# Performance work log

Hardware: AMD Instinct MI355X
Metric: run time of the kernel (lower is better)

The kernel has to match this reference:

```python
import jax, jax.numpy as jnp
import numpy as np

DIM = 768
HEADS = 8
HEAD_DIM = DIM // HEADS
SCALE = HEAD_DIM ** -0.5
EPS = 1e-5


def layernorm(x, gamma, beta):
    mu = jnp.mean(x, axis=-1, keepdims=True)
    var = jnp.mean((x - mu) ** 2, axis=-1, keepdims=True)
    return (x - mu) * jax.lax.rsqrt(var + EPS) * gamma + beta


def setup_inputs() -> dict:
    key = jax.random.key(0)
    ks = jax.random.split(key, 12)
    B, L, M, D = 8, 1024, 1024, DIM
    s = D ** -0.5
    return {
        "x": jax.random.normal(ks[0], (B, L, D), jnp.float32),
        "context": jax.random.normal(ks[1], (B, M, D), jnp.float32),
        "Wq": jax.random.normal(ks[2], (D, D), jnp.float32) * s,
        "bq": jnp.zeros((D,), jnp.float32),
        "Wkv": jax.random.normal(ks[3], (D, 2 * D), jnp.float32) * s,
        "bkv": jnp.zeros((2 * D,), jnp.float32),
        "Wp": jax.random.normal(ks[4], (D, D), jnp.float32) * s,
        "bp": jnp.zeros((D,), jnp.float32),
        "g1": jnp.ones((D,), jnp.float32),
        "b1": jnp.zeros((D,), jnp.float32),
        "g2": jnp.ones((D,), jnp.float32),
        "b2": jnp.zeros((D,), jnp.float32),
    }


def reference(x, context, Wq, bq, Wkv, bkv, Wp, bp, g1, b1, g2, b2):
    B, L, D = x.shape
    M = context.shape[1]
    Hp = Wp_ = int(L ** 0.5)
    x_n = layernorm(x, g1, b1)
    c_n = layernorm(context, g2, b2)
    q = (x_n @ Wq + bq).reshape(B, L, HEADS, HEAD_DIM).transpose(0, 2, 1, 3)  # bhld
    kv = (c_n @ Wkv + bkv).reshape(B, M, 2, HEADS, HEAD_DIM).transpose(2, 0, 3, 1, 4)
    k, v = kv[0], kv[1]  # bhmd
    attn = jnp.einsum("bhld,bhmd->bhlm", q, k) * SCALE
    w = jax.nn.softmax(attn, axis=-1)
    attn_map = w.mean(axis=1).sum(axis=-1).reshape(B, Hp, Wp_)
    out = jnp.einsum("bhlm,bhmd->bhld", w, v).transpose(0, 2, 1, 3).reshape(B, L, D)
    out = out @ Wp + bp
    # dropout is identity in eval mode (training=False)
    return out + x, attn_map
```

## Files before the change

kernel.cpp:

```cpp
#include <hip/hip_runtime.h>

typedef unsigned short u16;
typedef short bf16x8 __attribute__((ext_vector_type(8)));
typedef float f32x4 __attribute__((ext_vector_type(4)));
typedef unsigned short u16x8 __attribute__((ext_vector_type(8)));
typedef unsigned short u16x4 __attribute__((ext_vector_type(4)));

union bfr { unsigned int u[4]; bf16x8 v; };

__device__ __forceinline__ u16 f2bf(float f) {
    unsigned int u = __builtin_bit_cast(unsigned int, f);
    u = (u + 0x7fffu + ((u >> 16) & 1u)) >> 16;
    return (u16)u;
}

__device__ __forceinline__ unsigned int cvtpk(float lo, float hi) {
    unsigned int r;
    asm("v_cvt_pk_bf16_f32 %0, %1, %2" : "=v"(r) : "v"(lo), "v"(hi));
    return r;
}

__device__ __forceinline__ void gload16(const u16* src, u16* lds_dst) {
    __builtin_amdgcn_global_load_lds(
        (const __attribute__((address_space(1))) unsigned int*)src,
        (__attribute__((address_space(3))) unsigned int*)lds_dst, 16, 0, 0);
}

__global__ __launch_bounds__(256) void prep_ln_k(
    const float* __restrict__ x, const float* __restrict__ ctx,
    const float* __restrict__ g1, const float* __restrict__ b1,
    const float* __restrict__ g2, const float* __restrict__ b2,
    const float* __restrict__ Wq, const float* __restrict__ Wkv,
    const float* __restrict__ Wp,
    u16* __restrict__ xn, u16* __restrict__ cn,
    u16* __restrict__ WqT, u16* __restrict__ WkvT, u16* __restrict__ WpT)
{
    const int id = blockIdx.x;
    const int t = threadIdx.x;
    if (id >= 4096) {
        __shared__ float T[64][65];
        int t2 = id - 4096;
        const float* src; u16* dst; int lds, k0, n0;
        if (t2 < 288) { src = Wkv; dst = WkvT; lds = 1536; k0 = (t2 / 24) * 64; n0 = (t2 % 24) * 64; }
        else if (t2 < 432) { int u = t2 - 288; src = Wq; dst = WqT; lds = 768; k0 = (u / 12) * 64; n0 = (u % 12) * 64; }
        else { int u = t2 - 432; src = Wp; dst = WpT; lds = 768; k0 = (u / 12) * 64; n0 = (u % 12) * 64; }
        const int rr = t >> 4, c4 = (t & 15) * 4;
        #pragma unroll
        for (int it = 0; it < 4; it++) {
            int r = rr + it * 16;
            f32x4 v = *(const f32x4*)&src[(long)(k0 + r) * lds + n0 + c4];
            #pragma unroll
            for (int j = 0; j < 4; j++) T[c4 + j][r] = v[j];
        }
        __syncthreads();
        #pragma unroll
        for (int it = 0; it < 4; it++) {
            int r = rr + it * 16;
            u16x4 w;
            #pragma unroll
            for (int j = 0; j < 4; j++) w[j] = f2bf(T[r][c4 + j]);
            *(u16x4*)&dst[(long)(n0 + r) * 768 + k0 + c4] = w;
        }
        return;
    }
    const int lane = t & 63, w = t >> 6;
    const int row = id * 4 + w;
    const float* src; const float* g; const float* b; u16* dst;
    if (row < 8192) { src = x + (long)row * 768; g = g1; b = b1; dst = xn + (long)row * 768; }
    else { int r = row - 8192; src = ctx + (long)r * 768; g = g2; b = b2; dst = cn + (long)r * 768; }

    const int c0 = lane * 4;
    f32x4 v0 = *(const f32x4*)&src[c0];
    f32x4 v1 = *(const f32x4*)&src[c0 + 256];
    f32x4 v2 = *(const f32x4*)&src[c0 + 512];
    float s = (v0[0] + v0[1] + v0[2] + v0[3]) + (v1[0] + v1[1] + v1[2] + v1[3])
            + (v2[0] + v2[1] + v2[2] + v2[3]);
    #pragma unroll
    for (int o = 32; o; o >>= 1) s += __shfl_xor(s, o);
    const float mu = s * (1.0f / 768.0f);
    float q = 0.f;
    #pragma unroll
    for (int j = 0; j < 4; j++) { float d = v0[j] - mu; q += d * d; }
    #pragma unroll
    for (int j = 0; j < 4; j++) { float d = v1[j] - mu; q += d * d; }
    #pragma unroll
    for (int j = 0; j < 4; j++) { float d = v2[j] - mu; q += d * d; }
    #pragma unroll
    for (int o = 32; o; o >>= 1) q += __shfl_xor(q, o);
    const float rs = rsqrtf(q * (1.0f / 768.0f) + 1e-5f);

    f32x4 ga0 = *(const f32x4*)&g[c0],       ba0 = *(const f32x4*)&b[c0];
    f32x4 ga1 = *(const f32x4*)&g[c0 + 256], ba1 = *(const f32x4*)&b[c0 + 256];
    f32x4 ga2 = *(const f32x4*)&g[c0 + 512], ba2 = *(const f32x4*)&b[c0 + 512];
    u16x4 w0, w1, w2;
    #pragma unroll
    for (int j = 0; j < 4; j++) {
        w0[j] = f2bf((v0[j] - mu) * rs * ga0[j] + ba0[j]);
        w1[j] = f2bf((v1[j] - mu) * rs * ga1[j] + ba1[j]);
        w2[j] = f2bf((v2[j] - mu) * rs * ga2[j] + ba2[j]);
    }
    *(u16x4*)&dst[c0]       = w0;
    *(u16x4*)&dst[c0 + 256] = w1;
    *(u16x4*)&dst[c0 + 512] = w2;
}

__global__ __launch_bounds__(256) void qkv_k(
    const u16* __restrict__ xn, const u16* __restrict__ cn,
    const u16* __restrict__ WqT, const u16* __restrict__ WkvT,
    const float* __restrict__ bq, const float* __restrict__ bkv,
    u16* __restrict__ Qb, u16* __restrict__ Kb, u16* __restrict__ Vt)
{
    __shared__ u16 As[64 * 32];
    __shared__ u16 Bs[128 * 32];
    const int id = blockIdx.x;
    const int swz = (id & 7) * 288 + (id >> 3);
    const int tid = threadIdx.x, lane = tid & 63, wid = tid >> 6;
    const int wr = wid >> 1, wc = wid & 1;
    const int g = lane >> 4, i15 = lane & 15;

    const bool isQ = swz < 768;
    int rt, ct;
    const u16* A; const u16* Bt; const float* bias;
    if (isQ) { rt = swz / 6;  ct = swz % 6;  A = xn; Bt = WqT;  bias = bq; }
    else { int s2 = swz - 768; rt = s2 / 12; ct = s2 % 12; A = cn; Bt = WkvT; bias = bkv; }
    const int row0 = rt * 64, col0 = ct * 128;

    const u16* srcA; const u16* srcB[2]; int offA, offB[2];
    {
        int r = tid >> 2, sl = tid & 3;
        srcA = A + (long)(row0 + r) * 768 + ((sl ^ ((r >> 1) & 3)) << 3);
        offA = wid * 512 + lane * 8;
        #pragma unroll
        for (int c = 0; c < 2; c++) {
            int ch = c * 256 + tid;
            int rb = ch >> 2, slb = ch & 3;
            srcB[c] = Bt + (long)(col0 + rb) * 768 + ((slb ^ ((rb >> 1) & 3)) << 3);
            offB[c] = (c * 256 + wid * 64) * 8 + lane * 8;
        }
    }
    const int dA = wid * 512;
    int dB[2]; dB[0] = wid * 512; dB[1] = 2048 + wid * 512;

    int aoff[2], boff[4];
    #pragma unroll
    for (int m = 0; m < 2; m++) {
        int R = wr * 32 + m * 16 + i15;
        aoff[m] = R * 32 + ((g ^ ((R >> 1) & 3)) << 3);
    }
    #pragma unroll
    for (int n = 0; n < 4; n++) {
        int R = wc * 64 + n * 16 + i15;
        boff[n] = R * 32 + ((g ^ ((R >> 1) & 3)) << 3);
    }

    f32x4 acc[2][4] = {};
    for (int k0 = 0; k0 < 768; k0 += 32) {
        __syncthreads();
        gload16(srcA + k0, &As[dA]);
        #pragma unroll
        for (int c = 0; c < 2; c++)
            gload16(srcB[c] + k0, &Bs[dB[c]]);
        __syncthreads();
        bf16x8 av[2], bv[4];
        #pragma unroll
        for (int m = 0; m < 2; m++) av[m] = *(const bf16x8*)&As[aoff[m]];
        #pragma unroll
        for (int n = 0; n < 4; n++) bv[n] = *(const bf16x8*)&Bs[boff[n]];
        #pragma unroll
        for (int m = 0; m < 2; m++)
            #pragma unroll
            for (int n = 0; n < 4; n++)
                acc[m][n] = __builtin_amdgcn_mfma_f32_16x16x32_bf16(av[m], bv[n], acc[m][n], 0, 0, 0);
    }

    float bv4[4];
    #pragma unroll
    for (int n = 0; n < 4; n++) bv4[n] = bias[col0 + wc * 64 + n * 16 + i15];

    #pragma unroll
    for (int m = 0; m < 2; m++) {
        #pragma unroll
        for (int n = 0; n < 4; n++) {
            const int col = col0 + wc * 64 + n * 16 + i15;
            #pragma unroll
            for (int r = 0; r < 4; r++) {
                const int row = row0 + wr * 32 + m * 16 + g * 4 + r;
                float v = acc[m][n][r];
                if (isQ) {
                    v = (v + bv4[n]) * 0.14724444706f;
                    int b = row >> 10, l = row & 1023;
                    int h = col / 96, d = col % 96;
                    Qb[((long)(b * 8 + h) * 1024 + l) * 96 + d] = f2bf(v);
                } else {
                    v += bv4[n];
                    int b = row >> 10, mt = row & 1023;
                    if (col < 768) {
                        int h = col / 96, d = col % 96;
                        Kb[((long)(b * 8 + h) * 1024 + mt) * 96 + d] = f2bf(v);
                    } else {
                        int cc = col - 768;
                        int h = cc / 96, d = cc % 96;
                        Vt[((long)(b * 8 + h) * 96 + d) * 1024 + mt] = f2bf(v);
                    }
                }
            }
        }
    }
}

__global__ __launch_bounds__(256) void flash_k(
    const u16* __restrict__ Qb, const u16* __restrict__ Kb,
    const u16* __restrict__ Vt, u16* __restrict__ Ob)
{
    const int i = blockIdx.x;
    const int s8 = i >> 3;
    const int bh = (i & 7) * 8 + (s8 >> 4);
    const int qt = s8 & 15;
    const int tid = threadIdx.x, lane = tid & 63, wid = tid >> 6;
    const int g = lane >> 4, i15 = lane & 15;

    __shared__ u16 Ks[6144];
    __shared__ u16 Vs[2][6144];

    const long baseQK = (long)bh * 98304;
    const u16* Kt  = Kb + baseQK;
    const u16* Vtp = Vt + baseQK;

    bf16x8 qf[3];
    {
        const u16* qrow = Qb + baseQK + (long)(qt * 64 + wid * 16 + i15) * 96 + g * 8;
        qf[0] = *(const bf16x8*)(qrow);
        qf[1] = *(const bf16x8*)(qrow + 32);
        qf[2] = *(const bf16x8*)(qrow + 64);
    }

    int krd[4][3];
    #pragma unroll
    for (int n = 0; n < 4; n++) {
        int q4 = i15 >> 2, rr = i15 & 3, m = n >> 1;
        int R = (n & 1) ? (m * 32 + ((q4 ^ 2) << 3) + 4 + rr)
                        : (m * 32 + (q4 << 3) + rr);
        #pragma unroll
        for (int kd = 0; kd < 3; kd++)
            krd[n][kd] = kd * 2048 + R * 32 + ((g ^ ((R >> 3) & 3) ^ kd) << 3);
    }
    int vrd[6][2];
    #pragma unroll
    for (int n6 = 0; n6 < 6; n6++) {
        int row = n6 * 16 + i15;
        #pragma unroll
        for (int kk = 0; kk < 2; kk++)
            vrd[n6][kk] = row * 64 + ((kk * 32 + g * 8) ^ ((row & 7) << 3));
    }

    int kgo[3], kwr[3], vgo[3], vwr[3];
    #pragma unroll
    for (int it = 0; it < 3; it++) {
        int e = tid + it * 256;
        int r = e / 12, cEl = (e % 12) * 8;
        int kd = cEl >> 5, slot = (cEl >> 3) & 3;
        kgo[it] = r * 96 + cEl;
        kwr[it] = kd * 2048 + r * 32 + ((slot ^ ((r >> 3) & 3) ^ kd) << 3);
        int d = e >> 3, m8 = (e & 7) * 8;
        vgo[it] = d * 1024 + m8;
        vwr[it] = d * 64 + (m8 ^ ((d & 7) << 3));
    }

    u16x8 kreg[3], vreg[3];
    #pragma unroll
    for (int it = 0; it < 3; it++) {
        kreg[it] = *(const u16x8*)&Kt[kgo[it]];
        vreg[it] = *(const u16x8*)&Vtp[vgo[it]];
    }
    #pragma unroll
    for (int it = 0; it < 3; it++) {
        *(u16x8*)&Ks[kwr[it]] = kreg[it];
        *(u16x8*)&Vs[0][vwr[it]] = vreg[it];
    }

    f32x4 o[6] = {};
    float lsum = 0.f;
    int cur = 0;

    for (int t = 0; t < 16; t++) {
        __syncthreads();
        if (t < 15) {
            #pragma unroll
            for (int it = 0; it < 3; it++) {
                kreg[it] = *(const u16x8*)&Kt[(t + 1) * 6144 + kgo[it]];
                vreg[it] = *(const u16x8*)&Vtp[(t + 1) * 64 + vgo[it]];
            }
        }

        f32x4 s[4] = {};
        #pragma unroll
        for (int kd = 0; kd < 3; kd++) {
            #pragma unroll
            for (int n = 0; n < 4; n++) {
                bf16x8 kf = *(const bf16x8*)&Ks[krd[n][kd]];
                s[n] = __builtin_amdgcn_mfma_f32_16x16x32_bf16(kf, qf[kd], s[n], 0, 0, 0);
            }
        }
        __syncthreads();
        if (t < 15) {
            #pragma unroll
            for (int it = 0; it < 3; it++)
                *(u16x8*)&Ks[kwr[it]] = kreg[it];
        }

        unsigned int pk[4][2];
        #pragma unroll
        for (int n = 0; n < 4; n++) {
            float p0 = exp2f(s[n][0]), p1 = exp2f(s[n][1]);
            float p2 = exp2f(s[n][2]), p3 = exp2f(s[n][3]);
            lsum += (p0 + p1) + (p2 + p3);
            pk[n][0] = cvtpk(p0, p1);
            pk[n][1] = cvtpk(p2, p3);
        }

        #pragma unroll
        for (int kk = 0; kk < 2; kk++) {
            bfr pa;
            pa.u[0] = pk[kk * 2][0];
            pa.u[1] = pk[kk * 2][1];
            pa.u[2] = __shfl_xor(pk[kk * 2 + 1][0], 32);
            pa.u[3] = __shfl_xor(pk[kk * 2 + 1][1], 32);
            #pragma unroll
            for (int n6 = 0; n6 < 6; n6++) {
                bf16x8 vf = *(const bf16x8*)&Vs[cur][vrd[n6][kk]];
                o[n6] = __builtin_amdgcn_mfma_f32_16x16x32_bf16(pa.v, vf, o[n6], 0, 0, 0);
            }
        }

        if (t < 15) {
            #pragma unroll
            for (int it = 0; it < 3; it++)
                *(u16x8*)&Vs[cur ^ 1][vwr[it]] = vreg[it];
        }
        cur ^= 1;
    }

    lsum += __shfl_xor(lsum, 16);
    lsum += __shfl_xor(lsum, 32);
    float linv = 1.0f / lsum;

    const int b = bh >> 3, h = bh & 7;
    #pragma unroll
    for (int r = 0; r < 4; r++) {
        float lr = __shfl(linv, g * 4 + r);
        int row = qt * 64 + wid * 16 + g * 4 + r;
        long base = ((long)(b * 1024 + row)) * 768 + h * 96;
        #pragma unroll
        for (int n6 = 0; n6 < 6; n6++)
            Ob[base + n6 * 16 + i15] = f2bf(o[n6][r] * lr);
    }
}

__global__ __launch_bounds__(256) void out_k(
    const u16* __restrict__ Ob, const u16* __restrict__ WpT,
    const float* __restrict__ bp, const float* __restrict__ resid,
    float* __restrict__ out, float* __restrict__ amap)
{
    const int id = blockIdx.x;
    if (id >= 768) {
        amap[(id - 768) * 256 + threadIdx.x] = 1.0f;
        return;
    }
    __shared__ u16 As[64 * 32];
    __shared__ u16 Bs[128 * 32];
    const int swz = (id & 7) * 96 + (id >> 3);
    const int rt = swz / 6, ct = swz % 6;
    const int row0 = rt * 64, col0 = ct * 128;
    const int tid = threadIdx.x, lane = tid & 63, wid = tid >> 6;
    const int wr = wid >> 1, wc = wid & 1;
    const int g = lane >> 4, i15 = lane & 15;

    const u16* srcA; const u16* srcB[2];
    {
        int r = tid >> 2, sl = tid & 3;
        srcA = Ob + (long)(row0 + r) * 768 + ((sl ^ ((r >> 1) & 3)) << 3);
        #pragma unroll
        for (int c = 0; c < 2; c++) {
            int ch = c * 256 + tid;
            int rb = ch >> 2, slb = ch & 3;
            srcB[c] = WpT + (long)(col0 + rb) * 768 + ((slb ^ ((rb >> 1) & 3)) << 3);
        }
    }
    const int dA = wid * 512;
    int dB[2]; dB[0] = wid * 512; dB[1] = 2048 + wid * 512;

    int aoff[2], boff[4];
    #pragma unroll
    for (int m = 0; m < 2; m++) {
        int R = wr * 32 + m * 16 + i15;
        aoff[m] = R * 32 + ((g ^ ((R >> 1) & 3)) << 3);
    }
    #pragma unroll
    for (int n = 0; n < 4; n++) {
        int R = wc * 64 + n * 16 + i15;
        boff[n] = R * 32 + ((g ^ ((R >> 1) & 3)) << 3);
    }

    f32x4 acc[2][4] = {};
    for (int k0 = 0; k0 < 768; k0 += 32) {
        __syncthreads();
        gload16(srcA + k0, &As[dA]);
        #pragma unroll
        for (int c = 0; c < 2; c++)
            gload16(srcB[c] + k0, &Bs[dB[c]]);
        __syncthreads();
        bf16x8 av[2], bv[4];
        #pragma unroll
        for (int m = 0; m < 2; m++) av[m] = *(const bf16x8*)&As[aoff[m]];
        #pragma unroll
        for (int n = 0; n < 4; n++) bv[n] = *(const bf16x8*)&Bs[boff[n]];
        #pragma unroll
        for (int m = 0; m < 2; m++)
            #pragma unroll
            for (int n = 0; n < 4; n++)
                acc[m][n] = __builtin_amdgcn_mfma_f32_16x16x32_bf16(av[m], bv[n], acc[m][n], 0, 0, 0);
    }

    float bv4[4];
    #pragma unroll
    for (int n = 0; n < 4; n++) bv4[n] = bp[col0 + wc * 64 + n * 16 + i15];

    #pragma unroll
    for (int m = 0; m < 2; m++) {
        #pragma unroll
        for (int n = 0; n < 4; n++) {
            const int col = col0 + wc * 64 + n * 16 + i15;
            #pragma unroll
            for (int r = 0; r < 4; r++) {
                const int row = row0 + wr * 32 + m * 16 + g * 4 + r;
                long idx = (long)row * 768 + col;
                out[idx] = acc[m][n][r] + bv4[n] + resid[idx];
            }
        }
    }
}

extern "C" void kernel_launch(void* const* d_in, const int* in_sizes, int n_in,
                              void* d_out, int out_size, void* d_ws, size_t ws_size,
                              hipStream_t stream)
{
    const float* x   = (const float*)d_in[0];
    const float* ctx = (const float*)d_in[1];
    const float* Wq  = (const float*)d_in[2];
    const float* bq  = (const float*)d_in[3];
    const float* Wkv = (const float*)d_in[4];
    const float* bkv = (const float*)d_in[5];
    const float* Wp  = (const float*)d_in[6];
    const float* bp  = (const float*)d_in[7];
    const float* g1  = (const float*)d_in[8];
    const float* b1  = (const float*)d_in[9];
    const float* g2  = (const float*)d_in[10];
    const float* b2  = (const float*)d_in[11];
    float* out = (float*)d_out;

    char* w = (char*)d_ws;
    const long SZ_ROWS = 8192L * 768 * 2;
    long off = 0;
    u16* xn   = (u16*)(w + off); off += SZ_ROWS;
    u16* cn   = (u16*)(w + off); off += SZ_ROWS;
    u16* WqT  = (u16*)(w + off); off += 768L * 768 * 2;
    u16* WkvT = (u16*)(w + off); off += 1536L * 768 * 2;
    u16* WpT  = (u16*)(w + off); off += 768L * 768 * 2;
    u16* Qb   = (u16*)(w + off); off += SZ_ROWS;
    u16* Kb   = (u16*)(w + off); off += SZ_ROWS;
    u16* Vt   = (u16*)(w + off); off += SZ_ROWS;
    u16* Ob   = (u16*)(w + off); off += SZ_ROWS;

    prep_ln_k<<<4672, 256, 0, stream>>>(x, ctx, g1, b1, g2, b2, Wq, Wkv, Wp,
                                        xn, cn, WqT, WkvT, WpT);
    qkv_k<<<2304, 256, 0, stream>>>(xn, cn, WqT, WkvT, bq, bkv, Qb, Kb, Vt);
    flash_k<<<1024, 256, 0, stream>>>(Qb, Kb, Vt, Ob);
    out_k<<<800, 256, 0, stream>>>(Ob, WpT, bp, x, out, out + 6291456L);
}
```

Baseline: 162.1 us.

## Restructure QKV GEMM into independent per-wave 64x64 tiles with double-buffered LDS

Each wave now owns its own 64x64 output tile and private double-buffered LDS staging, so the block-wide __syncthreads barriers are gone and the next K-slice is prefetched with vmcnt waits while the current one is multiplied. The grid is halved, since each block now covers four wave tiles. The cost being targeted is barrier stalls and exposed global-to-LDS latency in the K loop. In exchange the waves no longer share A/B tiles, which raises per-wave global traffic and LDS footprint (64 KB per block) and may reduce occupancy.

```diff
diff --git a/kernel.cpp b/kernel.cpp
--- a/kernel.cpp
+++ b/kernel.cpp
@@ -110,81 +110,85 @@
     const float* __restrict__ bq, const float* __restrict__ bkv,
     u16* __restrict__ Qb, u16* __restrict__ Kb, u16* __restrict__ Vt)
 {
-    __shared__ u16 As[64 * 32];
-    __shared__ u16 Bs[128 * 32];
+    __shared__ u16 L[4][2][4096];
     const int id = blockIdx.x;
-    const int swz = (id & 7) * 288 + (id >> 3);
+    const int swz = (id & 7) * 144 + (id >> 3);
     const int tid = threadIdx.x, lane = tid & 63, wid = tid >> 6;
-    const int wr = wid >> 1, wc = wid & 1;
     const int g = lane >> 4, i15 = lane & 15;
 
-    const bool isQ = swz < 768;
-    int rt, ct;
-    const u16* A; const u16* Bt; const float* bias;
-    if (isQ) { rt = swz / 6;  ct = swz % 6;  A = xn; Bt = WqT;  bias = bq; }
-    else { int s2 = swz - 768; rt = s2 / 12; ct = s2 % 12; A = cn; Bt = WkvT; bias = bkv; }
-    const int row0 = rt * 64, col0 = ct * 128;
-
-    const u16* srcA; const u16* srcB[2]; int offA, offB[2];
-    {
-        int r = tid >> 2, sl = tid & 3;
-        srcA = A + (long)(row0 + r) * 768 + ((sl ^ ((r >> 1) & 3)) << 3);
-        offA = wid * 512 + lane * 8;
-        #pragma unroll
-        for (int c = 0; c < 2; c++) {
-            int ch = c * 256 + tid;
-            int rb = ch >> 2, slb = ch & 3;
-            srcB[c] = Bt + (long)(col0 + rb) * 768 + ((slb ^ ((rb >> 1) & 3)) << 3);
-            offB[c] = (c * 256 + wid * 64) * 8 + lane * 8;
-        }
-    }
-    const int dA = wid * 512;
-    int dB[2]; dB[0] = wid * 512; dB[1] = 2048 + wid * 512;
-
-    int aoff[2], boff[4];
-    #pragma unroll
-    for (int m = 0; m < 2; m++) {
-        int R = wr * 32 + m * 16 + i15;
-        aoff[m] = R * 32 + ((g ^ ((R >> 1) & 3)) << 3);
-    }
-    #pragma unroll
-    for (int n = 0; n < 4; n++) {
-        int R = wc * 64 + n * 16 + i15;
-        boff[n] = R * 32 + ((g ^ ((R >> 1) & 3)) << 3);
-    }
-
-    f32x4 acc[2][4] = {};
-    for (int k0 = 0; k0 < 768; k0 += 32) {
-        __syncthreads();
-        gload16(srcA + k0, &As[dA]);
-        #pragma unroll
-        for (int c = 0; c < 2; c++)
-            gload16(srcB[c] + k0, &Bs[dB[c]]);
-        __syncthreads();
-        bf16x8 av[2], bv[4];
-        #pragma unroll
-        for (int m = 0; m < 2; m++) av[m] = *(const bf16x8*)&As[aoff[m]];
-        #pragma unroll
-        for (int n = 0; n < 4; n++) bv[n] = *(const bf16x8*)&Bs[boff[n]];
-        #pragma unroll
-        for (int m = 0; m < 2; m++)
+    const int wt = swz * 4 + wid;
+    const int rt = wt / 36, c36 = wt % 36;
+    const bool isQ = c36 < 12;
+    const u16* A  = isQ ? xn : cn;
+    const u16* Bt = isQ ? WqT : WkvT;
+    const float* bias = isQ ? bq : bkv;
+    const int row0 = rt * 64;
+    const int col0 = (isQ ? c36 : (c36 - 12)) * 64;
+
+    const u16* srcA[4]; const u16* srcB[4];
+    #pragma unroll
+    for (int c = 0; c < 4; c++) {
+        int ch = c * 64 + lane;
+        int r = ch >> 2, sl = ch & 3;
+        int colx = ((sl ^ ((r >> 1) & 3)) << 3);
+        srcA[c] = A  + (long)(row0 + r) * 768 + colx;
+        srcB[c] = Bt + (long)(col0 + r) * 768 + colx;
+    }
+
+    int foff[4];
+    #pragma unroll
+    for (int m = 0; m < 4; m++) {
+        int R = m * 16 + i15;
+        foff[m] = R * 32 + ((g ^ ((R >> 1) & 3)) << 3);
+    }
+
+    f32x4 acc[4][4] = {};
+
+#define WSTAGE(BUF, T) do {                                              \
+    _Pragma("unroll")                                                    \
+    for (int c_ = 0; c_ < 4; c_++)                                       \
+        gload16(srcA[c_] + (T) * 32, &L[wid][BUF][c_ * 512]);            \
+    _Pragma("unroll")                                                    \
+    for (int c_ = 0; c_ < 4; c_++)                                       \
+        gload16(srcB[c_] + (T) * 32, &L[wid][BUF][2048 + c_ * 512]);     \
+} while (0)
+
+    WSTAGE(0, 0);
+    #pragma unroll
+    for (int t = 0; t < 24; t++) {
+        if (t + 1 < 24) {
+            WSTAGE((t + 1) & 1, t + 1);
+            asm volatile("s_waitcnt vmcnt(8)" ::: "memory");
+        } else {
+            asm volatile("s_waitcnt vmcnt(0)" ::: "memory");
+        }
+        __builtin_amdgcn_sched_barrier(0);
+        const u16* Lb = &L[wid][t & 1][0];
+        bf16x8 av[4], bv[4];
+        #pragma unroll
+        for (int m = 0; m < 4; m++) av[m] = *(const bf16x8*)&Lb[foff[m]];
+        #pragma unroll
+        for (int n = 0; n < 4; n++) bv[n] = *(const bf16x8*)&Lb[2048 + foff[n]];
+        #pragma unroll
+        for (int m = 0; m < 4; m++)
             #pragma unroll
             for (int n = 0; n < 4; n++)
                 acc[m][n] = __builtin_amdgcn_mfma_f32_16x16x32_bf16(av[m], bv[n], acc[m][n], 0, 0, 0);
     }
+#undef WSTAGE
 
     float bv4[4];
     #pragma unroll
-    for (int n = 0; n < 4; n++) bv4[n] = bias[col0 + wc * 64 + n * 16 + i15];
-
-    #pragma unroll
-    for (int m = 0; m < 2; m++) {
+    for (int n = 0; n < 4; n++) bv4[n] = bias[col0 + n * 16 + i15];
+
+    #pragma unroll
+    for (int m = 0; m < 4; m++) {
         #pragma unroll
         for (int n = 0; n < 4; n++) {
-            const int col = col0 + wc * 64 + n * 16 + i15;
+            const int col = col0 + n * 16 + i15;
             #pragma unroll
             for (int r = 0; r < 4; r++) {
-                const int row = row0 + wr * 32 + m * 16 + g * 4 + r;
+                const int row = row0 + m * 16 + g * 4 + r;
                 float v = acc[m][n][r];
                 if (isQ) {
                     v = (v + bv4[n]) * 0.14724444706f;
@@ -473,7 +477,7 @@
 
     prep_ln_k<<<4672, 256, 0, stream>>>(x, ctx, g1, b1, g2, b2, Wq, Wkv, Wp,
                                         xn, cn, WqT, WkvT, WpT);
-    qkv_k<<<2304, 256, 0, stream>>>(xn, cn, WqT, WkvT, bq, bkv, Qb, Kb, Vt);
+    qkv_k<<<1152, 256, 0, stream>>>(xn, cn, WqT, WkvT, bq, bkv, Qb, Kb, Vt);
     flash_k<<<1024, 256, 0, stream>>>(Qb, Kb, Vt, Ob);
     out_k<<<800, 256, 0, stream>>>(Ob, WpT, bp, x, out, out + 6291456L);
 }
```

Result: slower. 165.5 us (+2.1%).
